# Kernel optimization log

Measured on AMD Instinct MI355X. Metric: run time of the kernel, lower is better.

Reference implementation:

```python
import jax, jax.numpy as jnp
import numpy as np

NEG_FILL = -10000000.0  # matches torch masked_fill value


def setup_inputs() -> dict:
    key = jax.random.key(0)
    kq, kk, kv = jax.random.split(key, 3)
    B, H, S, D = 4, 16, 2048, 64
    Q = jax.random.normal(kq, (B, H, S, D), dtype=jnp.float32)
    K = jax.random.normal(kk, (B, H, S, D), dtype=jnp.float32)
    V = jax.random.normal(kv, (B, H, S, D), dtype=jnp.float32)
    return {"Q": Q, "K": K, "V": V}


def reference(Q, K, V):
    # Q,K,V: [B,H,S,D]
    D = K.shape[-1]
    scale = 1.0 / jnp.sqrt(jnp.asarray(D, dtype=Q.dtype))
    # scores: [B,H,S,S]
    scores = jnp.einsum("bhqd,bhkd->bhqk", Q, K) * scale
    S = scores.shape[-1]
    # causal mask: True above diagonal (future positions) -> filled with NEG_FILL
    causal = jnp.triu(jnp.ones((S, S), dtype=bool), k=1)
    scores = jnp.where(causal, jnp.asarray(NEG_FILL, dtype=scores.dtype), scores)
    attn = jax.nn.softmax(scores, axis=-1)
    return jnp.einsum("bhqk,bhkd->bhqd", attn, V)
```

## Files before the change

### kernel.cpp

```cpp
#include <hip/hip_runtime.h>
#include <hip/hip_bf16.h>


#define SEQ 2048
#define DIM 64
#define BH  64

typedef _Float16 half8  __attribute__((ext_vector_type(8)));
typedef _Float16 half4v __attribute__((ext_vector_type(4)));
typedef float    float4v __attribute__((ext_vector_type(4)));
typedef unsigned short ushort4v __attribute__((ext_vector_type(4)));

__device__ __forceinline__ void async16(const _Float16* g, _Float16* l) {
    __builtin_amdgcn_global_load_lds(
        (const __attribute__((address_space(1))) void*)g,
        (__attribute__((address_space(3))) void*)l, 16, 0, 0);
}

#if defined(__has_builtin)
#if __has_builtin(__builtin_elementwise_min)
#define EMIN4(a, b) __builtin_elementwise_min((a), (b))
#endif
#if __has_builtin(__builtin_amdgcn_exp2f)
#define EXP2F(x) __builtin_amdgcn_exp2f(x)
#endif
#endif
#ifndef EMIN4
__device__ __forceinline__ half4v emin4_fallback(half4v a, half4v b) {
    half4v r;
    r[0] = a[0] < b[0] ? a[0] : b[0];
    r[1] = a[1] < b[1] ? a[1] : b[1];
    r[2] = a[2] < b[2] ? a[2] : b[2];
    r[3] = a[3] < b[3] ? a[3] : b[3];
    return r;
}
#define EMIN4(a, b) emin4_fallback((a), (b))
#endif
#ifndef EXP2F
#define EXP2F(x) exp2f(x)
#endif

__global__ __launch_bounds__(256)
void prep_kernel(const float* __restrict__ K, const float* __restrict__ V,
                 _Float16* __restrict__ Kh, _Float16* __restrict__ Vt) {
    const int bid = blockIdx.x;
    const int tid = threadIdx.x;
    if (bid < 4096) {
        size_t idx = (size_t)bid * 2048 + (size_t)tid * 8;
        float4v a = *(const float4v*)(K + idx);
        float4v b = *(const float4v*)(K + idx + 4);
        half8 h;
        h[0] = (_Float16)a[0]; h[1] = (_Float16)a[1];
        h[2] = (_Float16)a[2]; h[3] = (_Float16)a[3];
        h[4] = (_Float16)b[0]; h[5] = (_Float16)b[1];
        h[6] = (_Float16)b[2]; h[7] = (_Float16)b[3];
        *(half8*)(Kh + idx) = h;
    } else {
        __shared__ _Float16 Vl[64 * 64];
        const int b  = bid - 4096;
        const int bh = b >> 5;
        const int s0 = (b & 31) * 64;
        {
            const int r   = tid >> 2;
            const int c16 = (tid & 3) * 16;
            const float* p = V + ((size_t)bh * SEQ + s0 + r) * DIM + c16;
            float4v x0 = *(const float4v*)(p);
            float4v x1 = *(const float4v*)(p + 4);
            float4v x2 = *(const float4v*)(p + 8);
            float4v x3 = *(const float4v*)(p + 12);
            half8 h0, h1;
            h0[0] = (_Float16)x0[0]; h0[1] = (_Float16)x0[1];
            h0[2] = (_Float16)x0[2]; h0[3] = (_Float16)x0[3];
            h0[4] = (_Float16)x1[0]; h0[5] = (_Float16)x1[1];
            h0[6] = (_Float16)x1[2]; h0[7] = (_Float16)x1[3];
            h1[0] = (_Float16)x2[0]; h1[1] = (_Float16)x2[1];
            h1[2] = (_Float16)x2[2]; h1[3] = (_Float16)x2[3];
            h1[4] = (_Float16)x3[0]; h1[5] = (_Float16)x3[1];
            h1[6] = (_Float16)x3[2]; h1[7] = (_Float16)x3[3];
            const int k  = (r + (r >> 3)) & 7;
            const int j0 = c16 >> 3;
            *(half8*)&Vl[r * 64 + ((j0    ) ^ k) * 8] = h0;
            *(half8*)&Vl[r * 64 + ((j0 + 1) ^ k) * 8] = h1;
        }
        __syncthreads();
        {
            const int d  = tid >> 2;
            const int sc = (tid & 3) * 16;
            const int dh = d >> 3;
            const int dl = d & 7;
            half8 o0, o1;
#pragma unroll
            for (int j = 0; j < 8; ++j) {
                const int s1 = sc + j;
                const int s2 = sc + 8 + j;
                o0[j] = Vl[s1 * 64 + ((dh ^ ((s1 + (s1 >> 3)) & 7)) << 3) + dl];
                o1[j] = Vl[s2 * 64 + ((dh ^ ((s2 + (s2 >> 3)) & 7)) << 3) + dl];
            }
            _Float16* op = Vt + ((size_t)bh * DIM + d) * SEQ + s0 + sc;
            *(half8*)op       = o0;
            *(half8*)(op + 8) = o1;
        }
    }
}

__global__ __launch_bounds__(128, 3)
void fa_main(const float* __restrict__ Q, const _Float16* __restrict__ Kh,
             const _Float16* __restrict__ Vt, float* __restrict__ O) {
    const int bid = blockIdx.x;
    const int xcd = bid & 7;
    const int r   = bid >> 3;
    const int bh  = xcd * 8 + (r & 7);
    const int t   = 31 - (r >> 3);

    const float*    Qb = Q  + (size_t)bh * SEQ * DIM;
    const _Float16* Kb = Kh + (size_t)bh * SEQ * DIM;
    const _Float16* Vb = Vt + (size_t)bh * DIM * SEQ;
    float*          Ob = O  + (size_t)bh * SEQ * DIM;

    const int tid  = threadIdx.x;
    const int wave = tid >> 6;
    const int lane = tid & 63;
    const int row  = lane & 15;
    const int quad = lane >> 4;

    __shared__ _Float16 Kl[2][64 * 64];
    __shared__ _Float16 Pl[2][32 * 64];

    const float SC = 0.125f * 1.44269504f;
    const float4v z0 = {0.f, 0.f, 0.f, 0.f};
    half8 ones;
    {
        ushort4v ob;
        ob[0] = 0x3c00; ob[1] = 0x3c00; ob[2] = 0x3c00; ob[3] = 0x3c00;
        half4v o1 = __builtin_bit_cast(half4v, ob);
        ones[0] = o1[0]; ones[1] = o1[1]; ones[2] = o1[2]; ones[3] = o1[3];
        ones[4] = o1[0]; ones[5] = o1[1]; ones[6] = o1[2]; ones[7] = o1[3];
    }
    half4v wcap;
    {
        ushort4v cb;
        cb[0] = 0x7400; cb[1] = 0x7400; cb[2] = 0x7400; cb[3] = 0x7400;
        wcap = __builtin_bit_cast(half4v, cb);
    }

#define STAGE_K(bsel, kt_)                                                      \
    {                                                                           \
        const _Float16* Kt0 = Kb + (size_t)(kt_) * 64 * DIM;                    \
        _Pragma("unroll")                                                       \
        for (int i = 0; i < 4; ++i) {                                           \
            int pos = wave * 256 + i * 64 + lane;                               \
            int rr  = pos >> 3;                                                 \
            int cc  = (pos & 7) ^ (rr & 7);                                     \
            async16(Kt0 + (size_t)rr * DIM + cc * 8,                            \
                    &Kl[bsel][0] + (size_t)(wave * 256 + i * 64) * 8);          \
        }                                                                       \
    }

    const int q0 = t * 64;

    half8 qf[4];
#pragma unroll
    for (int qs = 0; qs < 2; ++qs) {
        const float* qp = Qb + (size_t)(q0 + wave * 32 + qs * 16 + row) * DIM;
#pragma unroll
        for (int s = 0; s < 2; ++s) {
            const float* p = qp + s * 32 + quad * 8;
            float4v a = *(const float4v*)p;
            float4v b = *(const float4v*)(p + 4);
            half8 h;
            h[0] = (_Float16)(a[0] * SC); h[1] = (_Float16)(a[1] * SC);
            h[2] = (_Float16)(a[2] * SC); h[3] = (_Float16)(a[3] * SC);
            h[4] = (_Float16)(b[0] * SC); h[5] = (_Float16)(b[1] * SC);
            h[6] = (_Float16)(b[2] * SC); h[7] = (_Float16)(b[3] * SC);
            qf[qs * 2 + s] = h;
        }
    }

    float4v o_acc[2][4];
    float4v lacc[2];
#pragma unroll
    for (int qs = 0; qs < 2; ++qs) {
        float4v z = {0.f, 0.f, 0.f, 0.f};
        lacc[qs] = z;
#pragma unroll
        for (int c = 0; c < 4; ++c) o_acc[qs][c] = z;
    }

    STAGE_K(0, 0)
    __syncthreads();

    for (int kt = 0; kt <= t; ++kt) {
        const int cb = kt & 1;
        if (kt < t) STAGE_K(cb ^ 1, kt + 1)

        half8 vfr[4][2];
        {
            const _Float16* vp0 = Vb + (size_t)kt * 64 + quad * 8;
#pragma unroll
            for (int c = 0; c < 4; ++c) {
                const _Float16* vp = vp0 + (size_t)(c * 16 + row) * SEQ;
                vfr[c][0] = *(const half8*)(vp);
                vfr[c][1] = *(const half8*)(vp + 32);
            }
        }

        float4v sacc[2][4];
        __builtin_amdgcn_s_setprio(1);
#pragma unroll
        for (int c = 0; c < 4; ++c) {
            const int kv  = c * 16 + row;
            const int ch0 = quad ^ (row & 7);
            const int ch1 = (4 + quad) ^ (row & 7);
            half8 kf0 = *(const half8*)&Kl[cb][kv * 64 + ch0 * 8];
            half8 kf1 = *(const half8*)&Kl[cb][kv * 64 + ch1 * 8];
#pragma unroll
            for (int qs = 0; qs < 2; ++qs) {
                float4v s0 = __builtin_amdgcn_mfma_f32_16x16x32_f16(kf0, qf[qs * 2 + 0], z0, 0, 0, 0);
                sacc[qs][c] = __builtin_amdgcn_mfma_f32_16x16x32_f16(kf1, qf[qs * 2 + 1], s0, 0, 0, 0);
            }
        }
        __builtin_amdgcn_s_setprio(0);

        float pv[2][4][4];
        if (kt == t) {
#pragma unroll
            for (int qs = 0; qs < 2; ++qs) {
                const int ql = wave * 32 + qs * 16 + row;
#pragma unroll
                for (int c = 0; c < 4; ++c)
#pragma unroll
                    for (int rr = 0; rr < 4; ++rr) {
                        int kvl = c * 16 + quad * 4 + rr;
                        float sx = (kvl > ql) ? -1e30f : sacc[qs][c][rr];
                        pv[qs][c][rr] = EXP2F(sx);
                    }
            }
        } else {
#pragma unroll
            for (int qs = 0; qs < 2; ++qs)
#pragma unroll
                for (int c = 0; c < 4; ++c)
#pragma unroll
                    for (int rr = 0; rr < 4; ++rr)
                        pv[qs][c][rr] = EXP2F(sacc[qs][c][rr]);
        }

#pragma unroll
        for (int qs = 0; qs < 2; ++qs)
#pragma unroll
            for (int c = 0; c < 4; ++c) {
#if defined(__has_builtin) && __has_builtin(__builtin_amdgcn_cvt_pkrtz)
                auto t0 = __builtin_amdgcn_cvt_pkrtz(pv[qs][c][0], pv[qs][c][1]);
                auto t1 = __builtin_amdgcn_cvt_pkrtz(pv[qs][c][2], pv[qs][c][3]);
                half4v w;
                w[0] = t0[0]; w[1] = t0[1]; w[2] = t1[0]; w[3] = t1[1];
#else
                half4v w;
                w[0] = (_Float16)pv[qs][c][0]; w[1] = (_Float16)pv[qs][c][1];
                w[2] = (_Float16)pv[qs][c][2]; w[3] = (_Float16)pv[qs][c][3];
#endif
                w = EMIN4(w, wcap);
                const int jc  = c * 2 + (quad >> 1);
                const int col = ((jc ^ (row & 7)) << 3) + (quad & 1) * 4;
                *(half4v*)&Pl[wave][(qs * 16 + row) * 64 + col] = w;
            }
        asm volatile("s_waitcnt lgkmcnt(0)" ::: "memory");
        half8 af[2][2];
#pragma unroll
        for (int qs = 0; qs < 2; ++qs)
#pragma unroll
            for (int s = 0; s < 2; ++s) {
                const int js = (s * 4 + quad) ^ (row & 7);
                af[qs][s] = *(const half8*)&Pl[wave][(qs * 16 + row) * 64 + js * 8];
            }

        __builtin_amdgcn_s_setprio(1);
#pragma unroll
        for (int c = 0; c < 4; ++c)
#pragma unroll
            for (int s = 0; s < 2; ++s) {
                o_acc[0][c] = __builtin_amdgcn_mfma_f32_16x16x32_f16(vfr[c][s], af[0][s], o_acc[0][c], 0, 0, 0);
                o_acc[1][c] = __builtin_amdgcn_mfma_f32_16x16x32_f16(vfr[c][s], af[1][s], o_acc[1][c], 0, 0, 0);
            }
#pragma unroll
        for (int qs = 0; qs < 2; ++qs)
#pragma unroll
            for (int s = 0; s < 2; ++s)
                lacc[qs] = __builtin_amdgcn_mfma_f32_16x16x32_f16(ones, af[qs][s], lacc[qs], 0, 0, 0);
        __builtin_amdgcn_s_setprio(0);

        __syncthreads();
    }

#pragma unroll
    for (int qs = 0; qs < 2; ++qs) {
        const float inv = 1.0f / lacc[qs][0];
        float* op = Ob + (size_t)(q0 + wave * 32 + qs * 16 + row) * DIM + quad * 4;
#pragma unroll
        for (int c = 0; c < 4; ++c) {
            float4v o;
            o[0] = o_acc[qs][c][0] * inv; o[1] = o_acc[qs][c][1] * inv;
            o[2] = o_acc[qs][c][2] * inv; o[3] = o_acc[qs][c][3] * inv;
            *(float4v*)(op + c * 16) = o;
        }
    }
}

__global__ __launch_bounds__(256)
void fa_causal_fallback(const float* __restrict__ Q, const float* __restrict__ K,
                        const float* __restrict__ V, float* __restrict__ O) {
    const int bid = blockIdx.x;
    const int bh  = bid >> 5;
    const int qt  = bid & 31;
    const int q0  = qt * 64;

    const float* Qb = Q + (size_t)bh * SEQ * DIM;
    const float* Kb = K + (size_t)bh * SEQ * DIM;
    const float* Vb = V + (size_t)bh * SEQ * DIM;
    float*       Ob = O + (size_t)bh * SEQ * DIM;

    const int tid  = threadIdx.x;
    const int wave = tid >> 6;
    const int lane = tid & 63;
    const int row  = lane & 15;
    const int quad = lane >> 4;

    __shared__ _Float16 Kl[64][72];
    __shared__ _Float16 Vt[64][72];
    __shared__ _Float16 Pl[4][16][72];

    half8 qf[2];
    {
        const float* qp = Qb + (size_t)(q0 + wave * 16 + row) * DIM;
#pragma unroll
        for (int s = 0; s < 2; ++s) {
            const float* p = qp + s * 32 + quad * 8;
            float4v a = *(const float4v*)p;
            float4v b = *(const float4v*)(p + 4);
            half8 h;
            h[0] = (_Float16)a[0]; h[1] = (_Float16)a[1];
            h[2] = (_Float16)a[2]; h[3] = (_Float16)a[3];
            h[4] = (_Float16)b[0]; h[5] = (_Float16)b[1];
            h[6] = (_Float16)b[2]; h[7] = (_Float16)b[3];
            qf[s] = h;
        }
    }

    float m_i[4] = {-1e30f, -1e30f, -1e30f, -1e30f};
    float l_i[4] = {0.f, 0.f, 0.f, 0.f};
    float4v o_acc[4];
#pragma unroll
    for (int c = 0; c < 4; ++c) { float4v z = {0.f, 0.f, 0.f, 0.f}; o_acc[c] = z; }

    const float LOG2E = 1.44269504f;

    for (int kt = 0; kt <= qt; ++kt) {
        __syncthreads();
        {
            const int kvr = tid >> 2;
            const int c4  = tid & 3;
            const float* kp = Kb + (size_t)(kt * 64 + kvr) * DIM + c4 * 16;
            const float* vp = Vb + (size_t)(kt * 64 + kvr) * DIM + c4 * 16;
#pragma unroll
            for (int i = 0; i < 4; ++i) {
                float4v kx = *(const float4v*)(kp + i * 4);
                float4v vx = *(const float4v*)(vp + i * 4);
#pragma unroll
                for (int j = 0; j < 4; ++j) {
                    Kl[kvr][c4 * 16 + i * 4 + j] = (_Float16)kx[j];
                    Vt[c4 * 16 + i * 4 + j][kvr] = (_Float16)vx[j];
                }
            }
        }
        __syncthreads();

        float4v sacc[4];
#pragma unroll
        for (int c = 0; c < 4; ++c) { float4v z = {0.f, 0.f, 0.f, 0.f}; sacc[c] = z; }
#pragma unroll
        for (int c = 0; c < 4; ++c)
#pragma unroll
            for (int s = 0; s < 2; ++s) {
                half8 kf = *(const half8*)&Kl[c * 16 + row][s * 32 + quad * 8];
                sacc[c] = __builtin_amdgcn_mfma_f32_16x16x32_f16(qf[s], kf, sacc[c], 0, 0, 0);
            }

        float sv[4][4];
        const bool diag = (kt == qt);
#pragma unroll
        for (int c = 0; c < 4; ++c)
#pragma unroll
            for (int r = 0; r < 4; ++r) {
                float v = sacc[c][r] * 0.125f;
                if (diag) {
                    int kvl = c * 16 + row;
                    int ql  = wave * 16 + quad * 4 + r;
                    if (kvl > ql) v = -1e30f;
                }
                sv[c][r] = v;
            }

        float mnew[4], alpha[4];
#pragma unroll
        for (int r = 0; r < 4; ++r) {
            float rm = fmaxf(fmaxf(sv[0][r], sv[1][r]), fmaxf(sv[2][r], sv[3][r]));
            rm = fmaxf(rm, __shfl_xor(rm, 1));
            rm = fmaxf(rm, __shfl_xor(rm, 2));
            rm = fmaxf(rm, __shfl_xor(rm, 4));
            rm = fmaxf(rm, __shfl_xor(rm, 8));
            mnew[r]  = fmaxf(m_i[r], rm);
            alpha[r] = exp2f((m_i[r] - mnew[r]) * LOG2E);
            m_i[r]   = mnew[r];
        }
        float rs[4] = {0.f, 0.f, 0.f, 0.f};
#pragma unroll
        for (int c = 0; c < 4; ++c)
#pragma unroll
            for (int r = 0; r < 4; ++r) {
                float p = exp2f((sv[c][r] - mnew[r]) * LOG2E);
                sv[c][r] = p;
                rs[r] += p;
            }
#pragma unroll
        for (int r = 0; r < 4; ++r) {
            float s = rs[r];
            s += __shfl_xor(s, 1);
            s += __shfl_xor(s, 2);
            s += __shfl_xor(s, 4);
            s += __shfl_xor(s, 8);
            l_i[r] = l_i[r] * alpha[r] + s;
        }
#pragma unroll
        for (int c = 0; c < 4; ++c)
#pragma unroll
            for (int r = 0; r < 4; ++r)
                o_acc[c][r] *= alpha[r];

#pragma unroll
        for (int c = 0; c < 4; ++c)
#pragma unroll
            for (int r = 0; r < 4; ++r)
                Pl[wave][quad * 4 + r][c * 16 + row] = (_Float16)sv[c][r];
        __syncthreads();

        half8 af[2];
#pragma unroll
        for (int s = 0; s < 2; ++s)
            af[s] = *(const half8*)&Pl[wave][row][s * 32 + quad * 8];
#pragma unroll
        for (int c = 0; c < 4; ++c)
#pragma unroll
            for (int s = 0; s < 2; ++s) {
                half8 vf = *(const half8*)&Vt[c * 16 + row][s * 32 + quad * 8];
                o_acc[c] = __builtin_amdgcn_mfma_f32_16x16x32_f16(af[s], vf, o_acc[c], 0, 0, 0);
            }
    }

#pragma unroll
    for (int r = 0; r < 4; ++r) {
        float inv = 1.0f / l_i[r];
        float* op = Ob + (size_t)(q0 + wave * 16 + quad * 4 + r) * DIM;
#pragma unroll
        for (int c = 0; c < 4; ++c)
            op[c * 16 + row] = o_acc[c][r] * inv;
    }
}

extern "C" void kernel_launch(void* const* d_in, const int* in_sizes, int n_in,
                              void* d_out, int out_size, void* d_ws, size_t ws_size,
                              hipStream_t stream) {
    const float* Q = (const float*)d_in[0];
    const float* K = (const float*)d_in[1];
    const float* V = (const float*)d_in[2];
    float* O = (float*)d_out;

    const size_t elems = (size_t)BH * SEQ * DIM;
    const size_t need  = 2 * elems * sizeof(_Float16);

    if (ws_size >= need) {
        _Float16* Kh = (_Float16*)d_ws;
        _Float16* Vt = Kh + elems;
        prep_kernel<<<4096 + 2048, 256, 0, stream>>>(K, V, Kh, Vt);
        fa_main<<<BH * 32, 128, 0, stream>>>(Q, Kh, Vt, O);
    } else {
        fa_causal_fallback<<<BH * 32, 256, 0, stream>>>(Q, K, V, O);
    }
}
```

Before: 210.3 us.

## Stage V tiles into LDS via async loads instead of direct register loads

Each V tile is now loaded with async global-to-LDS copies into a swizzled shared buffer. The tile is then read from LDS just before the PV MFMAs, instead of being loaded straight from global memory into registers. A vmcnt wait plus barrier is added before the PV stage, and the launch-bounds occupancy hint drops from 3 to 2. This removes the long-lived V register fragments and moves the V fetch onto the async path, at the cost of an extra barrier per tile, more LDS use and lower occupancy. V is single-buffered, so the next iteration's staging may race with slow readers unless the trailing syncthreads covers it.

```diff
diff --git a/kernel.cpp b/kernel.cpp
--- a/kernel.cpp
+++ b/kernel.cpp
@@ -103,14 +103,14 @@
     }
 }
 
-__global__ __launch_bounds__(128, 3)
+__global__ __launch_bounds__(128, 2)
 void fa_main(const float* __restrict__ Q, const _Float16* __restrict__ Kh,
              const _Float16* __restrict__ Vt, float* __restrict__ O) {
     const int bid = blockIdx.x;
     const int xcd = bid & 7;
-    const int r   = bid >> 3;
-    const int bh  = xcd * 8 + (r & 7);
-    const int t   = 31 - (r >> 3);
+    const int idx = bid >> 3;
+    const int bh  = xcd * 8 + (idx & 7);
+    const int t   = 31 - (idx >> 3);
 
     const float*    Qb = Q  + (size_t)bh * SEQ * DIM;
     const _Float16* Kb = Kh + (size_t)bh * SEQ * DIM;
@@ -124,6 +124,7 @@
     const int quad = lane >> 4;
 
     __shared__ _Float16 Kl[2][64 * 64];
+    __shared__ _Float16 Vl[64 * 64];
     __shared__ _Float16 Pl[2][32 * 64];
 
     const float SC = 0.125f * 1.44269504f;
@@ -138,9 +139,9 @@
     }
     half4v wcap;
     {
-        ushort4v cb;
-        cb[0] = 0x7400; cb[1] = 0x7400; cb[2] = 0x7400; cb[3] = 0x7400;
-        wcap = __builtin_bit_cast(half4v, cb);
+        ushort4v cb2;
+        cb2[0] = 0x7400; cb2[1] = 0x7400; cb2[2] = 0x7400; cb2[3] = 0x7400;
+        wcap = __builtin_bit_cast(half4v, cb2);
     }
 
 #define STAGE_K(bsel, kt_)                                                      \
@@ -155,6 +156,18 @@
                     &Kl[bsel][0] + (size_t)(wave * 256 + i * 64) * 8);          \
         }                                                                       \
     }
+#define STAGE_V(kt_)                                                            \
+    {                                                                           \
+        const _Float16* Vt0 = Vb + (size_t)(kt_) * 64;                          \
+        _Pragma("unroll")                                                       \
+        for (int i = 0; i < 4; ++i) {                                           \
+            int pos = wave * 256 + i * 64 + lane;                               \
+            int rr  = pos >> 3;                                                 \
+            int cc  = (pos & 7) ^ (rr & 7);                                     \
+            async16(Vt0 + (size_t)rr * SEQ + cc * 8,                            \
+                    &Vl[0] + (size_t)(wave * 256 + i * 64) * 8);                \
+        }                                                                       \
+    }
 
     const int q0 = t * 64;
 
@@ -191,18 +204,8 @@
 
     for (int kt = 0; kt <= t; ++kt) {
         const int cb = kt & 1;
+        STAGE_V(kt)
         if (kt < t) STAGE_K(cb ^ 1, kt + 1)
-
-        half8 vfr[4][2];
-        {
-            const _Float16* vp0 = Vb + (size_t)kt * 64 + quad * 8;
-#pragma unroll
-            for (int c = 0; c < 4; ++c) {
-                const _Float16* vp = vp0 + (size_t)(c * 16 + row) * SEQ;
-                vfr[c][0] = *(const half8*)(vp);
-                vfr[c][1] = *(const half8*)(vp + 32);
-            }
-        }
 
         float4v sacc[2][4];
         __builtin_amdgcn_s_setprio(1);
@@ -274,14 +277,26 @@
                 af[qs][s] = *(const half8*)&Pl[wave][(qs * 16 + row) * 64 + js * 8];
             }
 
+        if (kt < t) {
+            asm volatile("s_waitcnt vmcnt(4)" ::: "memory");
+        } else {
+            asm volatile("s_waitcnt vmcnt(0)" ::: "memory");
+        }
+        __builtin_amdgcn_s_barrier();
+        __builtin_amdgcn_sched_barrier(0);
+
         __builtin_amdgcn_s_setprio(1);
 #pragma unroll
-        for (int c = 0; c < 4; ++c)
+        for (int c = 0; c < 4; ++c) {
+            const int d = c * 16 + row;
 #pragma unroll
             for (int s = 0; s < 2; ++s) {
-                o_acc[0][c] = __builtin_amdgcn_mfma_f32_16x16x32_f16(vfr[c][s], af[0][s], o_acc[0][c], 0, 0, 0);
-                o_acc[1][c] = __builtin_amdgcn_mfma_f32_16x16x32_f16(vfr[c][s], af[1][s], o_acc[1][c], 0, 0, 0);
-            }
+                const int ch = (s * 4 + quad) ^ (row & 7);
+                half8 vf = *(const half8*)&Vl[d * 64 + ch * 8];
+                o_acc[0][c] = __builtin_amdgcn_mfma_f32_16x16x32_f16(vf, af[0][s], o_acc[0][c], 0, 0, 0);
+                o_acc[1][c] = __builtin_amdgcn_mfma_f32_16x16x32_f16(vf, af[1][s], o_acc[1][c], 0, 0, 0);
+            }
+        }
 #pragma unroll
         for (int qs = 0; qs < 2; ++qs)
 #pragma unroll
```

Result: faster. 184.7 us (-12.2%).
